# Kernel tuning notes

Measured on AMD Instinct MI355X. Metric: run time of the kernel, lower is better.

Reference implementation:

```python
import jax, jax.numpy as jnp
import numpy as np

EMBED_DIM = 1024
CONTEXT_DIM = 768
NUM_HEADS = 16
HEAD_DIM = EMBED_DIM // NUM_HEADS
B, N, M = 8, 4096, 77


def setup_inputs() -> dict:
    key = jax.random.key(0)
    ks = jax.random.split(key, 12)
    s_in = 1.0 / np.sqrt(EMBED_DIM)
    s_ctx = 1.0 / np.sqrt(CONTEXT_DIM)
    x = jax.random.normal(ks[0], (B, N, EMBED_DIM), dtype=jnp.float32)
    context = jax.random.normal(ks[1], (B, M, CONTEXT_DIM), dtype=jnp.float32)
    # realistic padding mask: each example has a random valid prefix length in [1, M]
    lengths = jax.random.randint(ks[2], (B,), 1, M + 1)
    context_mask = jnp.arange(M)[None, :] < lengths[:, None]  # (B, M) bool
    Wq = jax.random.uniform(ks[3], (EMBED_DIM, EMBED_DIM), jnp.float32, -s_in, s_in)
    bq = jax.random.uniform(ks[4], (EMBED_DIM,), jnp.float32, -s_in, s_in)
    Wk = jax.random.uniform(ks[5], (CONTEXT_DIM, EMBED_DIM), jnp.float32, -s_ctx, s_ctx)
    bk = jax.random.uniform(ks[6], (EMBED_DIM,), jnp.float32, -s_ctx, s_ctx)
    Wv = jax.random.uniform(ks[7], (CONTEXT_DIM, EMBED_DIM), jnp.float32, -s_ctx, s_ctx)
    bv = jax.random.uniform(ks[8], (EMBED_DIM,), jnp.float32, -s_ctx, s_ctx)
    Wo = jax.random.uniform(ks[9], (EMBED_DIM, EMBED_DIM), jnp.float32, -s_in, s_in)
    bo = jax.random.uniform(ks[10], (EMBED_DIM,), jnp.float32, -s_in, s_in)
    return {"x": x, "context": context, "context_mask": context_mask,
            "Wq": Wq, "bq": bq, "Wk": Wk, "bk": bk, "Wv": Wv, "bv": bv,
            "Wo": Wo, "bo": bo}


def reference(x, context, context_mask, Wq, bq, Wk, bk, Wv, bv, Wo, bo):
    H, d = NUM_HEADS, HEAD_DIM
    scale = d ** -0.5
    Bx, Nx, _ = x.shape
    Mx = context.shape[1]
    # projections
    q = (x @ Wq + bq).reshape(Bx, Nx, H, d).transpose(0, 2, 1, 3)        # (B,H,N,d)
    k = (context @ Wk + bk).reshape(Bx, Mx, H, d).transpose(0, 2, 1, 3)  # (B,H,M,d)
    v = (context @ Wv + bv).reshape(Bx, Mx, H, d).transpose(0, 2, 1, 3)  # (B,H,M,d)
    # scores with padding mask
    attn = jnp.einsum('bhnd,bhmd->bhnm', q, k) * scale                   # (B,H,N,M)
    attn = jnp.where(context_mask[:, None, None, :], attn, -jnp.inf)
    attn = jax.nn.softmax(attn, axis=-1)
    out = jnp.einsum('bhnm,bhmd->bhnd', attn, v)                          # (B,H,N,d)
    out = out.transpose(0, 2, 1, 3).reshape(Bx, Nx, H * d)                # (B,N,E)
    return out @ Wo + bo
```

## Files before the change

### kernel.cpp

```cpp
#include <hip/hip_runtime.h>

typedef __bf16 bf16x8 __attribute__((ext_vector_type(8)));
typedef float f32x4 __attribute__((ext_vector_type(4)));

#define EMB 1024
#define CTXD 768
#define NH 16
#define HD 64
#define BB 8
#define NN 4096
#define MM 77
#define MPAD 96

static __device__ __forceinline__ unsigned short f2bf(float f) {
    unsigned u = __builtin_bit_cast(unsigned, f);
    u += 0x7FFFu + ((u >> 16) & 1u);
    return (unsigned short)(u >> 16);
}

__global__ void mask_lengths_kernel(const unsigned char* __restrict__ mask,
                                    int* __restrict__ lengths) {
    int ln = threadIdx.x & 63;
    int anyOdd = 0, anyF = 0;
    for (int i = ln; i < BB * MM; i += 64) {
        unsigned char v = mask[i];
        if (v == 0x80u || v == 0x3Fu) anyF = 1;
        if ((i & 3) && v) anyOdd = 1;
    }
    anyF = __any(anyF); anyOdd = __any(anyOdd);
    int layout = anyF ? 2 : (anyOdd ? 1 : 0);
    int b = ln >> 3, j = ln & 7, cnt = 0;
    for (int m = j; m < MM; m += 8) {
        int idx = b * MM + m;
        int valid;
        if (layout == 1)      valid = mask[idx] != 0;
        else if (layout == 0) valid = ((const int*)mask)[idx] != 0;
        else                  valid = ((const float*)mask)[idx] != 0.0f;
        cnt += valid ? 1 : 0;
    }
    cnt += __shfl_xor(cnt, 1, 64);
    cnt += __shfl_xor(cnt, 2, 64);
    cnt += __shfl_xor(cnt, 4, 64);
    if (j == 0) lengths[b] = cnt;
}

__global__ void cast_f32_to_bf16(const float* __restrict__ in,
                                 unsigned short* __restrict__ out, int n8) {
    for (int i = blockIdx.x * blockDim.x + threadIdx.x; i < n8;
         i += gridDim.x * blockDim.x) {
        float4 v0 = ((const float4*)in)[2 * i];
        float4 v1 = ((const float4*)in)[2 * i + 1];
        union { unsigned short u[8]; int4 v; } r;
        r.u[0] = f2bf(v0.x); r.u[1] = f2bf(v0.y);
        r.u[2] = f2bf(v0.z); r.u[3] = f2bf(v0.w);
        r.u[4] = f2bf(v1.x); r.u[5] = f2bf(v1.y);
        r.u[6] = f2bf(v1.z); r.u[7] = f2bf(v1.w);
        ((int4*)out)[i] = r.v;
    }
}

__global__ void cast_ctx_kernel(const float* __restrict__ in,
                                unsigned short* __restrict__ out) {
    int i = blockIdx.x * 256 + threadIdx.x;
    if (i >= 640 * CTXD / 8) return;
    int row = (i * 8) / CTXD;
    union { unsigned short u[8]; int4 v; } r;
    if (row < BB * MM) {
        float4 v0 = ((const float4*)in)[2 * i];
        float4 v1 = ((const float4*)in)[2 * i + 1];
        r.u[0] = f2bf(v0.x); r.u[1] = f2bf(v0.y);
        r.u[2] = f2bf(v0.z); r.u[3] = f2bf(v0.w);
        r.u[4] = f2bf(v1.x); r.u[5] = f2bf(v1.y);
        r.u[6] = f2bf(v1.z); r.u[7] = f2bf(v1.w);
    } else {
        r.v = make_int4(0, 0, 0, 0);
    }
    ((int4*)out)[i] = r.v;
}

struct TPtrs { const float* src[4]; unsigned short* dst[4]; };
__global__ void transpose4_kernel(TPtrs tp) {
    __shared__ float t[32][33];
    int z = blockIdx.z;
    int R = (z < 2) ? 1024 : 768, C = 1024;
    int r0 = blockIdx.y * 32;
    if (r0 >= R) return;
    const float* W = tp.src[z];
    unsigned short* Wt = tp.dst[z];
    int tx = threadIdx.x, ty = threadIdx.y;
    int c0 = blockIdx.x * 32;
#pragma unroll
    for (int i = 0; i < 32; i += 8)
        t[ty + i][tx] = W[(size_t)(r0 + ty + i) * C + c0 + tx];
    __syncthreads();
#pragma unroll
    for (int i = 0; i < 32; i += 8)
        Wt[(size_t)(c0 + ty + i) * R + r0 + tx] = f2bf(t[tx][ty + i]);
}

template <int MODE>
__global__ __launch_bounds__(512, 2) void gemm256_kernel(
    const unsigned short* __restrict__ A, const unsigned short* __restrict__ Bt,
    const float* __restrict__ bias, void* __restrict__ Cout,
    int M, int N, int K) {
    __shared__ unsigned short lds[4][2][256 * 32];
    const int tid = threadIdx.x, wv = tid >> 6, ln = tid & 63;
    const int numN = N >> 8;
    int bid = blockIdx.x;
    const int nwg = (M >> 8) * numN;
    if ((nwg & 7) == 0) { int cpx = nwg >> 3; bid = (bid & 7) * cpx + (bid >> 3); }
    const int nt_ = bid % numN, mt = bid / numN;
    const int m0 = mt << 8, n0 = nt_ << 8;
    const int wr = wv >> 2, wc = wv & 3;
    const int NT = K >> 5;

    const int srow = wv * 16 + (ln >> 2);
    const int sslot = ln & 3;

    f32x4 acc[8][4] = {};

#pragma unroll
    for (int t = 0; t < 3; ++t) {
#pragma unroll
        for (int half = 0; half < 2; ++half) {
            int row = half * 128 + srow;
            int gc = sslot ^ ((row >> 1) & 3);
            __builtin_amdgcn_global_load_lds(
                (const __attribute__((address_space(1))) void*)(
                    A + (size_t)(m0 + row) * K + (t << 5) + gc * 8),
                (__attribute__((address_space(3))) void*)(
                    &lds[t][0][(half * 128 + wv * 16) * 32]),
                16, 0, 0);
            __builtin_amdgcn_global_load_lds(
                (const __attribute__((address_space(1))) void*)(
                    Bt + (size_t)(n0 + row) * K + (t << 5) + gc * 8),
                (__attribute__((address_space(3))) void*)(
                    &lds[t][1][(half * 128 + wv * 16) * 32]),
                16, 0, 0);
        }
    }
    asm volatile("s_waitcnt vmcnt(8)" ::: "memory");
    __builtin_amdgcn_sched_barrier(0);
    __builtin_amdgcn_s_barrier();

    for (int t = 0; t < NT; ++t) {
        const unsigned short* As = lds[t & 3][0];
        const unsigned short* Bs = lds[t & 3][1];
        const int kt3 = (t + 3) << 5;
        if (t + 3 < NT) {
#pragma unroll
            for (int half = 0; half < 2; ++half) {
                int row = half * 128 + srow;
                int gc = sslot ^ ((row >> 1) & 3);
                __builtin_amdgcn_global_load_lds(
                    (const __attribute__((address_space(1))) void*)(
                        A + (size_t)(m0 + row) * K + kt3 + gc * 8),
                    (__attribute__((address_space(3))) void*)(
                        &lds[(t + 3) & 3][0][(half * 128 + wv * 16) * 32]),
                    16, 0, 0);
            }
        }
        bf16x8 bfr[4], af[4];
#pragma unroll
        for (int j = 0; j < 4; ++j) {
            int brow = wc * 64 + j * 16 + (ln & 15);
            int bslot = (ln >> 4) ^ ((brow >> 1) & 3);
            bfr[j] = *(const bf16x8*)(Bs + brow * 32 + bslot * 8);
        }
#pragma unroll
        for (int i = 0; i < 4; ++i) {
            int arow = wr * 128 + i * 16 + (ln & 15);
            int aslot = (ln >> 4) ^ ((arow >> 1) & 3);
            af[i] = *(const bf16x8*)(As + arow * 32 + aslot * 8);
        }
        __builtin_amdgcn_s_barrier();
        __builtin_amdgcn_s_setprio(1);
#pragma unroll
        for (int i = 0; i < 4; ++i)
#pragma unroll
            for (int j = 0; j < 4; ++j)
                acc[i][j] = __builtin_amdgcn_mfma_f32_16x16x32_bf16(
                    af[i], bfr[j], acc[i][j], 0, 0, 0);
        __builtin_amdgcn_s_setprio(0);
        __builtin_amdgcn_s_barrier();
        if (t + 3 < NT) {
#pragma unroll
            for (int half = 0; half < 2; ++half) {
                int row = half * 128 + srow;
                int gc = sslot ^ ((row >> 1) & 3);
                __builtin_amdgcn_global_load_lds(
                    (const __attribute__((address_space(1))) void*)(
                        Bt + (size_t)(n0 + row) * K + kt3 + gc * 8),
                    (__attribute__((address_space(3))) void*)(
                        &lds[(t + 3) & 3][1][(half * 128 + wv * 16) * 32]),
                    16, 0, 0);
            }
        }
#pragma unroll
        for (int i = 0; i < 4; ++i) {
            int arow = wr * 128 + (i + 4) * 16 + (ln & 15);
            int aslot = (ln >> 4) ^ ((arow >> 1) & 3);
            af[i] = *(const bf16x8*)(As + arow * 32 + aslot * 8);
        }
        __builtin_amdgcn_s_barrier();
        __builtin_amdgcn_s_setprio(1);
#pragma unroll
        for (int i = 0; i < 4; ++i)
#pragma unroll
            for (int j = 0; j < 4; ++j)
                acc[i + 4][j] = __builtin_amdgcn_mfma_f32_16x16x32_bf16(
                    af[i], bfr[j], acc[i + 4][j], 0, 0, 0);
        __builtin_amdgcn_s_setprio(0);
        if (t < NT - 1) {
            if (t + 3 < NT)      { asm volatile("s_waitcnt vmcnt(8)" ::: "memory"); }
            else if (t + 2 < NT) { asm volatile("s_waitcnt vmcnt(4)" ::: "memory"); }
            else                 { asm volatile("s_waitcnt vmcnt(0)" ::: "memory"); }
            __builtin_amdgcn_sched_barrier(0);
        }
        __builtin_amdgcn_s_barrier();
    }

    float bvals[4];
#pragma unroll
    for (int j = 0; j < 4; ++j)
        bvals[j] = bias[n0 + wc * 64 + j * 16 + (ln & 15)];
#pragma unroll
    for (int i = 0; i < 8; ++i)
#pragma unroll
        for (int j = 0; j < 4; ++j)
#pragma unroll
            for (int r = 0; r < 4; ++r) {
                int row = m0 + wr * 128 + i * 16 + (ln >> 4) * 4 + r;
                int col = n0 + wc * 64 + j * 16 + (ln & 15);
                float v = acc[i][j][r] + bvals[j];
                if constexpr (MODE == 0)
                    ((unsigned short*)Cout)[(size_t)row * N + col] = f2bf(v);
                else
                    ((float*)Cout)[(size_t)row * N + col] = v;
            }
}

static __device__ __forceinline__ void stage_tile(
    const unsigned short* __restrict__ G, int ldg, unsigned short* lds,
    int r0, int kt, int wv, int ln) {
    int rown = ln >> 2;
    int koff = (ln & 3) * 8;
#pragma unroll
    for (int r = 0; r < 2; ++r) {
        int cw = wv * 2 + r;
        const unsigned short* src =
            G + (size_t)(r0 + cw * 16 + rown) * ldg + kt + koff;
        __builtin_amdgcn_global_load_lds(
            (const __attribute__((address_space(1))) void*)src,
            (__attribute__((address_space(3))) void*)(lds + cw * 512),
            16, 0, 0);
    }
}

template <int MODE>
__global__ __launch_bounds__(256) void gemm_bt_kernel(
    const unsigned short* __restrict__ A, const unsigned short* __restrict__ Bt,
    const float* __restrict__ bias, void* __restrict__ Cout,
    int M, int N, int K) {
    __shared__ unsigned short As[128 * 32];
    __shared__ unsigned short Bs[128 * 32];
    const int tid = threadIdx.x, wv = tid >> 6, ln = tid & 63;
    const int numM = M >> 7, numN = N >> 7;
    int bid = blockIdx.x;
    const int nwg = numM * numN;
    if ((nwg & 7) == 0) { int cpx = nwg >> 3; bid = (bid & 7) * cpx + (bid >> 3); }
    const int nt = bid % numN, mt = bid / numN;
    const int m0 = mt << 7, n0 = nt << 7;
    const int wr = wv >> 1, wc = wv & 1;

    f32x4 acc[4][4] = {};
    for (int kt = 0; kt < K; kt += 32) {
        __syncthreads();
        stage_tile(A, K, As, m0, kt, wv, ln);
        stage_tile(Bt, K, Bs, n0, kt, wv, ln);
        __syncthreads();
        bf16x8 af[4], bfr[4];
#pragma unroll
        for (int i = 0; i < 4; ++i)
            af[i] = *(const bf16x8*)(As + (wr * 64 + i * 16 + (ln & 15)) * 32 +
                                     (ln >> 4) * 8);
#pragma unroll
        for (int j = 0; j < 4; ++j)
            bfr[j] = *(const bf16x8*)(Bs + (wc * 64 + j * 16 + (ln & 15)) * 32 +
                                      (ln >> 4) * 8);
#pragma unroll
        for (int i = 0; i < 4; ++i)
#pragma unroll
            for (int j = 0; j < 4; ++j)
                acc[i][j] = __builtin_amdgcn_mfma_f32_16x16x32_bf16(
                    af[i], bfr[j], acc[i][j], 0, 0, 0);
    }

    float bvals[4];
#pragma unroll
    for (int j = 0; j < 4; ++j)
        bvals[j] = bias[n0 + wc * 64 + j * 16 + (ln & 15)];

#pragma unroll
    for (int i = 0; i < 4; ++i) {
#pragma unroll
        for (int j = 0; j < 4; ++j) {
#pragma unroll
            for (int r = 0; r < 4; ++r) {
                int row = m0 + wr * 64 + i * 16 + (ln >> 4) * 4 + r;
                int col = n0 + wc * 64 + j * 16 + (ln & 15);
                float v = acc[i][j][r] + bvals[j];
                if (row < BB * MM) {
                    int bb = row / MM, m = row - bb * MM;
                    int hh = col >> 6, d = col & 63;
                    if constexpr (MODE == 2)
                        ((unsigned short*)Cout)[((size_t)(bb * NH + hh) * MPAD + m) * HD + d] = f2bf(v);
                    else
                        ((unsigned short*)Cout)[((size_t)(bb * NH + hh) * HD + d) * MPAD + m] = f2bf(v);
                }
            }
        }
    }
}

__global__ __launch_bounds__(256, 3) void attn_kernel(
    const unsigned short* __restrict__ Q, const unsigned short* __restrict__ Kw,
    const unsigned short* __restrict__ Vt, const int* __restrict__ lengths,
    unsigned short* __restrict__ Out) {
    const int bh = blockIdx.y;
    const int b = bh >> 4, h = bh & 15;
    const int q0 = blockIdx.x * 128;
    const int tid = threadIdx.x, wv = tid >> 6, ln = tid & 63;
    const int len = lengths[b];
    const int kscnt = (len + 31) >> 5;

    __shared__ unsigned short Ps[128][104];

    const unsigned short* Ksrc = Kw + (size_t)bh * (MPAD * HD);
    const unsigned short* Vsrc = Vt + (size_t)bh * (HD * MPAD);

    bf16x8 aq[2][2];
#pragma unroll
    for (int qi = 0; qi < 2; ++qi) {
        const int qr = q0 + wv * 32 + qi * 16 + (ln & 15);
        const unsigned short* qptr =
            Q + (size_t)(b * NN + qr) * EMB + h * HD + (ln >> 4) * 8;
        aq[qi][0] = *(const bf16x8*)(qptr);
        aq[qi][1] = *(const bf16x8*)(qptr + 32);
    }

    bf16x8 vf[3][4];
#pragma unroll
    for (int j = 0; j < 4; ++j)
        vf[0][j] = *(const bf16x8*)(Vsrc + (j * 16 + (ln & 15)) * MPAD +
                                    (ln >> 4) * 8);
    if (kscnt > 1) {
#pragma unroll
        for (int j = 0; j < 4; ++j)
            vf[1][j] = *(const bf16x8*)(Vsrc + (j * 16 + (ln & 15)) * MPAD + 32 +
                                        (ln >> 4) * 8);
    }
    if (kscnt > 2) {
#pragma unroll
        for (int j = 0; j < 4; ++j)
            vf[2][j] = *(const bf16x8*)(Vsrc + (j * 16 + (ln & 15)) * MPAD + 64 +
                                        (ln >> 4) * 8);
    }

    f32x4 s[2][5] = {};
#pragma unroll
    for (int t = 0; t < 5; ++t) {
        if (t * 16 < len) {
            const unsigned short* kp =
                Ksrc + (t * 16 + (ln & 15)) * HD + (ln >> 4) * 8;
            bf16x8 k0 = *(const bf16x8*)(kp);
            bf16x8 k1 = *(const bf16x8*)(kp + 32);
#pragma unroll
            for (int qi = 0; qi < 2; ++qi) {
                s[qi][t] = __builtin_amdgcn_mfma_f32_16x16x32_bf16(
                    aq[qi][0], k0, s[qi][t], 0, 0, 0);
                s[qi][t] = __builtin_amdgcn_mfma_f32_16x16x32_bf16(
                    aq[qi][1], k1, s[qi][t], 0, 0, 0);
            }
        }
    }

    const float scale = 0.125f;
    float mx[2][4], sum[2][4];
#pragma unroll
    for (int qi = 0; qi < 2; ++qi)
#pragma unroll
        for (int r = 0; r < 4; ++r) { mx[qi][r] = -1e30f; sum[qi][r] = 0.f; }
#pragma unroll
    for (int t = 0; t < 5; ++t) {
        int m = t * 16 + (ln & 15);
        bool valid = m < len;
#pragma unroll
        for (int qi = 0; qi < 2; ++qi)
#pragma unroll
            for (int r = 0; r < 4; ++r) {
                float v = valid ? s[qi][t][r] * scale : -1e30f;
                s[qi][t][r] = v;
                mx[qi][r] = fmaxf(mx[qi][r], v);
            }
    }
#pragma unroll
    for (int d = 1; d < 16; d <<= 1)
#pragma unroll
        for (int qi = 0; qi < 2; ++qi)
#pragma unroll
            for (int r = 0; r < 4; ++r)
                mx[qi][r] = fmaxf(mx[qi][r], __shfl_xor(mx[qi][r], d, 64));
#pragma unroll
    for (int t = 0; t < 5; ++t)
#pragma unroll
        for (int qi = 0; qi < 2; ++qi)
#pragma unroll
            for (int r = 0; r < 4; ++r) {
                float p = __expf(s[qi][t][r] - mx[qi][r]);
                s[qi][t][r] = p;
                sum[qi][r] += p;
            }
#pragma unroll
    for (int d = 1; d < 16; d <<= 1)
#pragma unroll
        for (int qi = 0; qi < 2; ++qi)
#pragma unroll
            for (int r = 0; r < 4; ++r)
                sum[qi][r] += __shfl_xor(sum[qi][r], d, 64);

    float rinv[2][4];
#pragma unroll
    for (int qi = 0; qi < 2; ++qi)
#pragma unroll
        for (int r = 0; r < 4; ++r) rinv[qi][r] = 1.0f / sum[qi][r];

#pragma unroll
    for (int t = 0; t < 6; ++t)
#pragma unroll
        for (int qi = 0; qi < 2; ++qi)
#pragma unroll
            for (int r = 0; r < 4; ++r) {
                int row = wv * 32 + qi * 16 + (ln >> 4) * 4 + r;
                float v = (t < 5) ? s[qi][t][r] * rinv[qi][r] : 0.0f;
                Ps[row][t * 16 + (ln & 15)] = f2bf(v);
            }

    f32x4 o[2][4] = {};
    for (int ks = 0; ks < kscnt; ++ks) {
#pragma unroll
        for (int qi = 0; qi < 2; ++qi) {
            bf16x8 pf = *(const bf16x8*)(&Ps[wv * 32 + qi * 16 + (ln & 15)]
                                            [ks * 32 + (ln >> 4) * 8]);
#pragma unroll
            for (int j = 0; j < 4; ++j)
                o[qi][j] = __builtin_amdgcn_mfma_f32_16x16x32_bf16(
                    vf[ks][j], pf, o[qi][j], 0, 0, 0);
        }
    }

#pragma unroll
    for (int qi = 0; qi < 2; ++qi) {
        const int qrow = q0 + wv * 32 + qi * 16 + (ln & 15);
        unsigned short* obase =
            Out + (size_t)(b * NN + qrow) * EMB + h * HD + (ln >> 4) * 4;
#pragma unroll
        for (int j = 0; j < 4; ++j) {
            union { unsigned short u[4]; unsigned long long ll; } pk;
#pragma unroll
            for (int r = 0; r < 4; ++r) pk.u[r] = f2bf(o[qi][j][r]);
            *(unsigned long long*)(obase + j * 16) = pk.ll;
        }
    }
}

extern "C" void kernel_launch(void* const* d_in, const int* in_sizes, int n_in,
                              void* d_out, int out_size, void* d_ws, size_t ws_size,
                              hipStream_t stream) {
    const float* x    = (const float*)d_in[0];
    const float* ctx  = (const float*)d_in[1];
    const unsigned char* cmask = (const unsigned char*)d_in[2];
    const float* Wq = (const float*)d_in[3];
    const float* bq = (const float*)d_in[4];
    const float* Wk = (const float*)d_in[5];
    const float* bk = (const float*)d_in[6];
    const float* Wv = (const float*)d_in[7];
    const float* bv = (const float*)d_in[8];
    const float* Wo = (const float*)d_in[9];
    const float* bo = (const float*)d_in[10];

    char* ws = (char*)d_ws;
    unsigned short* Xbf   = (unsigned short*)(ws);
    unsigned short* Wq_t  = (unsigned short*)(ws + 67108864);
    unsigned short* Wo_t  = (unsigned short*)(ws + 69206016);
    unsigned short* Wk_t  = (unsigned short*)(ws + 71303168);
    unsigned short* Wv_t  = (unsigned short*)(ws + 72876032);
    unsigned short* Cbf   = (unsigned short*)(ws + 74448896);
    unsigned short* Kw    = (unsigned short*)(ws + 75431936);
    unsigned short* Vtw   = (unsigned short*)(ws + 77004800);
    int* lengths          = (int*)(ws + 78577664);
    unsigned short* Qb    = (unsigned short*)d_out;

    mask_lengths_kernel<<<1, 64, 0, stream>>>(cmask, lengths);
    cast_f32_to_bf16<<<2048, 256, 0, stream>>>(x, Xbf, (BB * NN * EMB) / 8);
    cast_ctx_kernel<<<240, 256, 0, stream>>>(ctx, Cbf);
    TPtrs tp;
    tp.src[0] = Wq; tp.src[1] = Wo; tp.src[2] = Wk; tp.src[3] = Wv;
    tp.dst[0] = Wq_t; tp.dst[1] = Wo_t; tp.dst[2] = Wk_t; tp.dst[3] = Wv_t;
    transpose4_kernel<<<dim3(32, 32, 4), dim3(32, 8), 0, stream>>>(tp);
    hipMemsetAsync(Kw, 0, 2 * 1572864, stream);

    gemm256_kernel<0><<<512, 512, 0, stream>>>(Xbf, Wq_t, bq, Qb, 32768, 1024, 1024);
    gemm_bt_kernel<2><<<40, 256, 0, stream>>>(Cbf, Wk_t, bk, Kw, 640, 1024, 768);
    gemm_bt_kernel<3><<<40, 256, 0, stream>>>(Cbf, Wv_t, bv, Vtw, 640, 1024, 768);

    attn_kernel<<<dim3(32, 128), 256, 0, stream>>>(Qb, Kw, Vtw, lengths, Xbf);

    gemm256_kernel<1><<<512, 512, 0, stream>>>(Xbf, Wo_t, bo, d_out, 32768, 1024, 1024);
}
```

Baseline: 319.4 us.

## Prefetch next k-tile LDS fragments into registers during current MFMA phase

```diff
diff --git a/kernel.cpp b/kernel.cpp
--- a/kernel.cpp
+++ b/kernel.cpp
@@ -117,10 +117,7 @@
     const int srow = wv * 16 + (ln >> 2);
     const int sslot = ln & 3;
 
-    f32x4 acc[8][4] = {};
-
-#pragma unroll
-    for (int t = 0; t < 3; ++t) {
+    auto stageA = [&](int t) {
 #pragma unroll
         for (int half = 0; half < 2; ++half) {
             int row = half * 128 + srow;
@@ -129,50 +126,54 @@
                 (const __attribute__((address_space(1))) void*)(
                     A + (size_t)(m0 + row) * K + (t << 5) + gc * 8),
                 (__attribute__((address_space(3))) void*)(
-                    &lds[t][0][(half * 128 + wv * 16) * 32]),
+                    &lds[t & 3][0][(half * 128 + wv * 16) * 32]),
                 16, 0, 0);
+        }
+    };
+    auto stageB = [&](int t) {
+#pragma unroll
+        for (int half = 0; half < 2; ++half) {
+            int row = half * 128 + srow;
+            int gc = sslot ^ ((row >> 1) & 3);
             __builtin_amdgcn_global_load_lds(
                 (const __attribute__((address_space(1))) void*)(
                     Bt + (size_t)(n0 + row) * K + (t << 5) + gc * 8),
                 (__attribute__((address_space(3))) void*)(
-                    &lds[t][1][(half * 128 + wv * 16) * 32]),
+                    &lds[t & 3][1][(half * 128 + wv * 16) * 32]),
                 16, 0, 0);
         }
-    }
-    asm volatile("s_waitcnt vmcnt(8)" ::: "memory");
+    };
+    auto readA = [&](const unsigned short* As, int i) -> bf16x8 {
+        int arow = wr * 128 + i * 16 + (ln & 15);
+        int aslot = (ln >> 4) ^ ((arow >> 1) & 3);
+        return *(const bf16x8*)(As + arow * 32 + aslot * 8);
+    };
+    auto readB = [&](const unsigned short* Bs, int j) -> bf16x8 {
+        int brow = wc * 64 + j * 16 + (ln & 15);
+        int bslot = (ln >> 4) ^ ((brow >> 1) & 3);
+        return *(const bf16x8*)(Bs + brow * 32 + bslot * 8);
+    };
+
+    f32x4 acc[8][4] = {};
+    bf16x8 afA[4], afB[4], bfrC[4], afN[4], bfrN[4];
+
+    stageA(0); stageB(0); stageA(1); stageB(1); stageA(2); stageB(2);
+    asm volatile("s_waitcnt vmcnt(4)" ::: "memory");
     __builtin_amdgcn_sched_barrier(0);
     __builtin_amdgcn_s_barrier();
-
+#pragma unroll
+    for (int i = 0; i < 4; ++i) afA[i] = readA(lds[0][0], i);
+#pragma unroll
+    for (int j = 0; j < 4; ++j) bfrC[j] = readB(lds[0][1], j);
+
+#pragma unroll 4
     for (int t = 0; t < NT; ++t) {
         const unsigned short* As = lds[t & 3][0];
-        const unsigned short* Bs = lds[t & 3][1];
-        const int kt3 = (t + 3) << 5;
-        if (t + 3 < NT) {
-#pragma unroll
-            for (int half = 0; half < 2; ++half) {
-                int row = half * 128 + srow;
-                int gc = sslot ^ ((row >> 1) & 3);
-                __builtin_amdgcn_global_load_lds(
-                    (const __attribute__((address_space(1))) void*)(
-                        A + (size_t)(m0 + row) * K + kt3 + gc * 8),
-                    (__attribute__((address_space(3))) void*)(
-                        &lds[(t + 3) & 3][0][(half * 128 + wv * 16) * 32]),
-                    16, 0, 0);
-            }
-        }
-        bf16x8 bfr[4], af[4];
-#pragma unroll
-        for (int j = 0; j < 4; ++j) {
-            int brow = wc * 64 + j * 16 + (ln & 15);
-            int bslot = (ln >> 4) ^ ((brow >> 1) & 3);
-            bfr[j] = *(const bf16x8*)(Bs + brow * 32 + bslot * 8);
-        }
-#pragma unroll
-        for (int i = 0; i < 4; ++i) {
-            int arow = wr * 128 + i * 16 + (ln & 15);
-            int aslot = (ln >> 4) ^ ((arow >> 1) & 3);
-            af[i] = *(const bf16x8*)(As + arow * 32 + aslot * 8);
-        }
+        const unsigned short* Asn = lds[(t + 1) & 3][0];
+        const unsigned short* Bsn = lds[(t + 1) & 3][1];
+        if (t + 3 < NT) stageA(t + 3);
+#pragma unroll
+        for (int i = 0; i < 4; ++i) afB[i] = readA(As, i + 4);
         __builtin_amdgcn_s_barrier();
         __builtin_amdgcn_s_setprio(1);
 #pragma unroll
@@ -180,28 +181,19 @@
 #pragma unroll
             for (int j = 0; j < 4; ++j)
                 acc[i][j] = __builtin_amdgcn_mfma_f32_16x16x32_bf16(
-                    af[i], bfr[j], acc[i][j], 0, 0, 0);
+                    afA[i], bfrC[j], acc[i][j], 0, 0, 0);
         __builtin_amdgcn_s_setprio(0);
         __builtin_amdgcn_s_barrier();
-        if (t + 3 < NT) {
-#pragma unroll
-            for (int half = 0; half < 2; ++half) {
-                int row = half * 128 + srow;
-                int gc = sslot ^ ((row >> 1) & 3);
-                __builtin_amdgcn_global_load_lds(
-                    (const __attribute__((address_space(1))) void*)(
-                        Bt + (size_t)(n0 + row) * K + kt3 + gc * 8),
-                    (__attribute__((address_space(3))) void*)(
-                        &lds[(t + 3) & 3][1][(half * 128 + wv * 16) * 32]),
-                    16, 0, 0);
-            }
-        }
-#pragma unroll
-        for (int i = 0; i < 4; ++i) {
-            int arow = wr * 128 + (i + 4) * 16 + (ln & 15);
-            int aslot = (ln >> 4) ^ ((arow >> 1) & 3);
-            af[i] = *(const bf16x8*)(As + arow * 32 + aslot * 8);
-        }
+        if (t + 3 < NT) stageB(t + 3);
+        if (t + 1 < NT) {
+#pragma unroll
+            for (int i = 0; i < 4; ++i) afN[i] = readA(Asn, i);
+#pragma unroll
+            for (int j = 0; j < 4; ++j) bfrN[j] = readB(Bsn, j);
+        }
+        if (t + 3 < NT) { asm volatile("s_waitcnt vmcnt(4)" ::: "memory"); }
+        else            { asm volatile("s_waitcnt vmcnt(0)" ::: "memory"); }
+        __builtin_amdgcn_sched_barrier(0);
         __builtin_amdgcn_s_barrier();
         __builtin_amdgcn_s_setprio(1);
 #pragma unroll
@@ -209,15 +201,13 @@
 #pragma unroll
             for (int j = 0; j < 4; ++j)
                 acc[i + 4][j] = __builtin_amdgcn_mfma_f32_16x16x32_bf16(
-                    af[i], bfr[j], acc[i + 4][j], 0, 0, 0);
+                    afB[i], bfrC[j], acc[i + 4][j], 0, 0, 0);
         __builtin_amdgcn_s_setprio(0);
-        if (t < NT - 1) {
-            if (t + 3 < NT)      { asm volatile("s_waitcnt vmcnt(8)" ::: "memory"); }
-            else if (t + 2 < NT) { asm volatile("s_waitcnt vmcnt(4)" ::: "memory"); }
-            else                 { asm volatile("s_waitcnt vmcnt(0)" ::: "memory"); }
-            __builtin_amdgcn_sched_barrier(0);
-        }
         __builtin_amdgcn_s_barrier();
+#pragma unroll
+        for (int i = 0; i < 4; ++i) afA[i] = afN[i];
+#pragma unroll
+        for (int j = 0; j < 4; ++j) bfrC[j] = bfrN[j];
     }
 
     float bvals[4];
```

New measurement: 326.5 us. 1.02x slower.
